# Kernel optimization log

Measured on AMD Instinct MI355X. Metric: run time of the kernel, lower is better.

## Reference

```python
import jax, jax.numpy as jnp
import numpy as np

# config
BSZ, L_, DM = 4, 2048, 1024
H, G, P, N, R = 16, 4, 64, 64, 2
RATIO = H // G            # 4
E, K = 64, 2              # kmoe experts / top_k
DPROJ = H * P * 2 + G * N * R * 2 + G * 3  # 3084


def rms(x, w, eps=1e-5):
    return x * jax.lax.rsqrt(jnp.mean(x * x, axis=-1, keepdims=True) + eps) * w


def kron_moe(x, router_w, A_e, B_e, scale, bias, d1, d2, o1, o2, k):
    # x: [..., d1*d2] -> [..., o1*o2]
    orig = x.shape
    xf = x.reshape(-1, d1 * d2)
    logits = xf @ router_w.T                       # [T, E]
    vals, idx = jax.lax.top_k(logits, k)           # [T, k]
    probs = jax.nn.softmax(vals, axis=-1)
    xs = xf.reshape(-1, d1, d2)
    # Y[t,k,o,p] = sum_ij A[t,k,o,i] x[t,i,j] B[t,k,p,j]
    Y = jnp.einsum('tkoi,tij,tkpj->tkop', A_e[idx], xs, B_e[idx])
    out = jnp.sum(Y * probs[:, :, None, None], axis=1).reshape(orig[:-1] + (o1 * o2,))
    return out * scale + bias


def setup_inputs() -> dict:
    key = jax.random.key(0)
    ks = jax.random.split(key, 12)
    r = lambda k, s, sc: jax.random.normal(k, s, jnp.float32) * sc
    return dict(
        u=jax.random.normal(ks[0], (BSZ, L_, DM), jnp.float32),
        in_proj_w=r(ks[1], (DPROJ, DM), 0.02),
        in_proj_b=jnp.zeros((DPROJ,), jnp.float32),
        xup_router=r(ks[2], (E, P), 0.02),
        xup_A=r(ks[3], (E, 8, 8), 0.1),
        xup_B=r(ks[4], (E, 16, 8), 0.1),
        xup_scale=jnp.ones((1,), jnp.float32),
        xup_bias=jnp.zeros((P * R,), jnp.float32),
        ydown_w=r(ks[5], (P, P * R), 0.02),
        oup_router=r(ks[6], (E, H * P), 0.02),
        oup_A=r(ks[7], (E, 32, 32), 0.05),
        oup_B=r(ks[8], (E, 32, 32), 0.05),
        oup_scale=jnp.ones((1,), jnp.float32),
        oup_bias=jnp.zeros((DM,), jnp.float32),
        theta_log=r(ks[9], (G, N // 2), 1.0),
        D=jnp.ones((H,), jnp.float32),
        normB_w=jnp.ones((N * R,), jnp.float32),
        normC_w=jnp.ones((N * R,), jnp.float32),
        bias_B=jnp.zeros((G, N, R), jnp.float32),
        bias_C=jnp.zeros((G, N, R), jnp.float32),
        pregate_w=jnp.ones((H * P,), jnp.float32),
    )


def reference(u, in_proj_w, in_proj_b, xup_router, xup_A, xup_B, xup_scale, xup_bias,
              ydown_w, oup_router, oup_A, oup_B, oup_scale, oup_bias,
              theta_log, D, normB_w, normC_w, bias_B, bias_C, pregate_w):
    B, L, _ = u.shape
    HP, GNR = H * P, G * N * R
    proj = u @ in_proj_w.T + in_proj_b
    splits = np.cumsum([HP, HP, GNR, GNR, G, G])
    z, x_p, Bp, Cp, dt, A_p, lam = jnp.split(proj, splits, axis=-1)
    dt = jax.nn.softplus(dt)                       # [B,L,G]
    A = -jnp.exp(A_p)                              # [B,L,G]
    theta = jnp.exp(theta_log)                     # [G,N/2]
    Bp = rms(Bp.reshape(B, L, G, N * R), normB_w).reshape(B, L, G, N, R) + bias_B
    Cp = rms(Cp.reshape(B, L, G, N * R), normC_w).reshape(B, L, G, N, R) + bias_C
    angles_g = jnp.cumsum(dt[..., None] * theta[None, None], axis=1)   # [B,L,G,N/2]
    rep = lambda v: jnp.repeat(v, RATIO, axis=2)   # group -> head broadcast
    angles = rep(angles_g)                         # [B,L,H,N/2]
    dt_h = rep(dt[..., None])                      # [B,L,H,1]
    A_h = rep(A[..., None])                        # [B,L,H,1]
    B_h, C_h = rep(Bp), rep(Cp)                    # [B,L,H,N,R]
    cos = jnp.cos(angles)[..., None]
    sin = jnp.sin(angles)[..., None]

    def rotate(v):
        re, im = v[..., 0::2, :], v[..., 1::2, :]
        return jnp.stack([re * cos - im * sin, re * sin + im * cos], axis=-2).reshape(v.shape)

    B_rot, C_rot = rotate(B_h), rotate(C_h)
    x = kron_moe(x_p.reshape(B, L, H, P), xup_router, xup_A, xup_B, xup_scale, xup_bias,
                 8, 8, 8, 16, K).reshape(B, L, H, P, R)
    alpha = jnp.exp(dt_h * A_h)[..., None]         # [B,L,H,1,1]

    mv = lambda v: jnp.moveaxis(v, 1, 0)           # time-major for scan

    def step(h, xs):
        Br, Cr, xt, at, dtt = xs
        in_sig = jnp.einsum('bhnr,bhpr->bhnp', Br, xt)
        h = h * at + dtt[..., None] * in_sig
        y_t = jnp.einsum('bhnp,bhnr->bhpr', h, Cr)
        return h, y_t

    h0 = jnp.zeros((B, H, N, P), u.dtype)
    _, ys = jax.lax.scan(step, h0, (mv(B_rot), mv(C_rot), mv(x), mv(alpha), mv(dt_h)))
    y = jnp.moveaxis(ys, 0, 1)                     # [B,L,H,P,R]
    y = (y.reshape(B, L, H, P * R) @ ydown_w.T).reshape(B, L, H * P)
    y = rms(y + x_p * jnp.repeat(D, P), pregate_w) * jax.nn.sigmoid(z)
    out = kron_moe(y, oup_router, oup_A, oup_B, oup_scale, oup_bias, 32, 32, 32, 32, K)
    return out
```

## Files before the change

kernel.cpp:

```cpp
#include <hip/hip_runtime.h>
#include <hip/hip_bf16.h>
#include <math.h>

namespace {
constexpr int kB = 4, kL = 2048, kDM = 1024;
constexpr int kH = 16, kG = 4;
constexpr int kDPROJ = 3084;
constexpr int COL_Z = 0, COL_XP = 1024, COL_B = 2048, COL_C = 2560, COL_DT = 3072, COL_A = 3076;
constexpr int kTOK = kB * kL;
constexpr int kNC = kL / 64;
constexpr int kNPAD = 3200;
constexpr float kLOG2E = 1.4426950408889634f;
}

typedef __attribute__((ext_vector_type(8))) __bf16 bf16x8;
typedef __attribute__((ext_vector_type(8))) unsigned short u16x8;
typedef __attribute__((ext_vector_type(4))) float f32x4;

#define GLDS16(gp, lp)                                                          \
  __builtin_amdgcn_global_load_lds(                                             \
      (const __attribute__((address_space(1))) void*)(gp),                      \
      (__attribute__((address_space(3))) void*)(lp), 16, 0, 0)

__device__ __forceinline__ unsigned short bf16_rne(float f) {
  unsigned u = __builtin_bit_cast(unsigned, f);
  unsigned r = u + 0x7fffu + ((u >> 16) & 1u);
  return (unsigned short)(r >> 16);
}
__device__ __forceinline__ void split2(float f, unsigned short& h, unsigned short& l) {
  unsigned short hh = bf16_rne(f);
  float hf = __builtin_bit_cast(float, (unsigned)hh << 16);
  h = hh;
  l = bf16_rne(f - hf);
}
__device__ __forceinline__ bf16x8 ldsb8(const unsigned short* p) {
  return __builtin_bit_cast(bf16x8, *(const u16x8*)p);
}

__global__ __launch_bounds__(256) void k_split_u(const float* __restrict__ X,
                                                 unsigned short* __restrict__ hi,
                                                 unsigned short* __restrict__ lo) {
  int i = blockIdx.x * 256 + threadIdx.x;
  float4 x = ((const float4*)X)[i];
  float xs[4] = {x.x, x.y, x.z, x.w};
  ushort4 hv, lv;
  unsigned short hq[4], lq[4];
#pragma unroll
  for (int q = 0; q < 4; ++q) split2(xs[q], hq[q], lq[q]);
  hv.x = hq[0]; hv.y = hq[1]; hv.z = hq[2]; hv.w = hq[3];
  lv.x = lq[0]; lv.y = lq[1]; lv.z = lq[2]; lv.w = lq[3];
  ((ushort4*)hi)[i] = hv;
  ((ushort4*)lo)[i] = lv;
}

__global__ __launch_bounds__(256) void k_split_w(const float* __restrict__ X,
                                                 unsigned short* __restrict__ hi,
                                                 unsigned short* __restrict__ lo) {
  int i = blockIdx.x * 256 + threadIdx.x;
  int row = i >> 8;
  float4 x = make_float4(0.f, 0.f, 0.f, 0.f);
  if (row < kDPROJ) x = ((const float4*)X)[i];
  float xs[4] = {x.x, x.y, x.z, x.w};
  ushort4 hv, lv;
  unsigned short hq[4], lq[4];
#pragma unroll
  for (int q = 0; q < 4; ++q) split2(xs[q], hq[q], lq[q]);
  hv.x = hq[0]; hv.y = hq[1]; hv.z = hq[2]; hv.w = hq[3];
  lv.x = lq[0]; lv.y = lq[1]; lv.z = lq[2]; lv.w = lq[3];
  ((ushort4*)hi)[i] = hv;
  ((ushort4*)lo)[i] = lv;
}

__global__ __launch_bounds__(256) void k_inproj_mfma(
    const unsigned short* __restrict__ Uhi, const unsigned short* __restrict__ Ulo,
    const unsigned short* __restrict__ Whi, const unsigned short* __restrict__ Wlo,
    const float* __restrict__ bias, float* __restrict__ proj,
    float* __restrict__ dtA) {
  __shared__ unsigned short lds_u[16384];
  const int tid = threadIdx.x;
  const int wave = tid >> 6, lane = tid & 63;
  const int wm = wave >> 1, wn = wave & 1;
  const int row0 = blockIdx.x * 128, col0 = blockIdx.y * 128;
  const int fr = lane & 15, kq = lane >> 4;

  f32x4 acc[4][4];
#pragma unroll
  for (int i = 0; i < 4; ++i)
#pragma unroll
    for (int j = 0; j < 4; ++j) acc[i][j] = (f32x4){0.f, 0.f, 0.f, 0.f};

  const int s0 = wave * 64 + lane;

  for (int k0 = 0; k0 < kDM; k0 += 32) {
#pragma unroll
    for (int q = 0; q < 2; ++q) {
      const int slot = q * 256 + s0;
      const int r = slot >> 2;
      const int ce = ((slot & 3) ^ ((r >> 1) & 3)) * 8;
      const size_t ao = (size_t)(row0 + r) * kDM + k0 + ce;
      const size_t bo = (size_t)(col0 + r) * kDM + k0 + ce;
      const int lb = (q * 256 + wave * 64) * 16;
      GLDS16(Uhi + ao, (char*)lds_u + lb);
      GLDS16(Ulo + ao, (char*)lds_u + 8192 + lb);
      GLDS16(Whi + bo, (char*)lds_u + 16384 + lb);
      GLDS16(Wlo + bo, (char*)lds_u + 24576 + lb);
    }
    __syncthreads();
    bf16x8 ahi[4], alo[4], bhi[4], blo[4];
#pragma unroll
    for (int mi = 0; mi < 4; ++mi) {
      int r = wm * 64 + mi * 16 + fr;
      int off = r * 32 + ((kq ^ ((r >> 1) & 3)) * 8);
      ahi[mi] = ldsb8(lds_u + off);
      alo[mi] = ldsb8(lds_u + 4096 + off);
    }
#pragma unroll
    for (int ni = 0; ni < 4; ++ni) {
      int r = wn * 64 + ni * 16 + fr;
      int off = r * 32 + ((kq ^ ((r >> 1) & 3)) * 8);
      bhi[ni] = ldsb8(lds_u + 8192 + off);
      blo[ni] = ldsb8(lds_u + 12288 + off);
    }
#pragma unroll
    for (int mi = 0; mi < 4; ++mi)
#pragma unroll
      for (int ni = 0; ni < 4; ++ni) {
        acc[mi][ni] = __builtin_amdgcn_mfma_f32_16x16x32_bf16(ahi[mi], bhi[ni], acc[mi][ni], 0, 0, 0);
        acc[mi][ni] = __builtin_amdgcn_mfma_f32_16x16x32_bf16(ahi[mi], blo[ni], acc[mi][ni], 0, 0, 0);
        acc[mi][ni] = __builtin_amdgcn_mfma_f32_16x16x32_bf16(alo[mi], bhi[ni], acc[mi][ni], 0, 0, 0);
      }
    __syncthreads();
  }

  const int orow = row0 + wm * 64, ocol = col0 + wn * 64;
#pragma unroll
  for (int mi = 0; mi < 4; ++mi)
#pragma unroll
    for (int ni = 0; ni < 4; ++ni) {
      int cg = ocol + ni * 16 + fr;
      if (cg < kDPROJ) {
        float bv = bias[cg];
#pragma unroll
        for (int r = 0; r < 4; ++r) {
          int rg = orow + mi * 16 + kq * 4 + r;
          float v = acc[mi][ni][r] + bv;
          proj[(size_t)rg * kDPROJ + cg] = v;
          if (cg >= COL_DT && cg < COL_DT + 8)
            dtA[(size_t)rg * 8 + (cg - COL_DT)] = v;
        }
      }
    }
}

__global__ __launch_bounds__(256) void k_dtprep(const float* __restrict__ dtA,
                                                float* __restrict__ dtg,
                                                float* __restrict__ cumalog,
                                                double* __restrict__ cumdt) {
  int bg = blockIdx.x;
  int b = bg / kG, g = bg % kG;
  int tid = threadIdx.x;
  __shared__ double s_dt[256], s_al[256];
  double loc_dt[8], loc_al[8];
  double sdt = 0.0, sal = 0.0;
#pragma unroll
  for (int q = 0; q < 8; ++q) {
    int t = tid * 8 + q;
    size_t i = (size_t)(b * kL + t) * 8;
    float rd = dtA[i + g];
    float ra = dtA[i + 4 + g];
    float dt = rd > 20.f ? rd : log1pf(expf(rd));
    float al = -expf(ra) * dt;
    dtg[(size_t)(b * kL + t) * kG + g] = dt;
    sdt += (double)dt; loc_dt[q] = sdt;
    sal += (double)al; loc_al[q] = sal;
  }
  s_dt[tid] = sdt; s_al[tid] = sal;
  __syncthreads();
  for (int off = 1; off < 256; off <<= 1) {
    double a = 0.0, c = 0.0;
    if (tid >= off) { a = s_dt[tid - off]; c = s_al[tid - off]; }
    __syncthreads();
    s_dt[tid] += a; s_al[tid] += c;
    __syncthreads();
  }
  double base_dt = tid ? s_dt[tid - 1] : 0.0;
  double base_al = tid ? s_al[tid - 1] : 0.0;
#pragma unroll
  for (int q = 0; q < 8; ++q) {
    int t = tid * 8 + q;
    size_t idx = (size_t)(b * kL + t) * kG + g;
    cumdt[idx] = base_dt + loc_dt[q];
    cumalog[idx] = (float)(base_al + loc_al[q]);
  }
}

__global__ __launch_bounds__(256) void k_angles(const double* __restrict__ cumdt,
                                                const float* __restrict__ theta_log,
                                                float* __restrict__ cs_tab) {
  int idx = blockIdx.x * 256 + threadIdx.x;
  int tok = idx >> 7, gk = idx & 127, g = gk >> 5, k = gk & 31;
  double theta = exp((double)theta_log[g * 32 + k]);
  double ang = theta * cumdt[(size_t)tok * kG + g];
  const double twopi = 6.283185307179586476925286766559;
  double rem = ang - floor(ang / twopi) * twopi;
  cs_tab[(size_t)idx * 2] = cosf((float)rem);
  cs_tab[(size_t)idx * 2 + 1] = sinf((float)rem);
}

__global__ __launch_bounds__(1024) void k_rotate(float* __restrict__ proj,
                                                 const float* __restrict__ cs_tab,
                                                 const float* __restrict__ normB_w,
                                                 const float* __restrict__ normC_w,
                                                 const float* __restrict__ bias_B,
                                                 const float* __restrict__ bias_C) {
  int tok = blockIdx.x;
  int tid = threadIdx.x;
  __shared__ float buf[1024];
  __shared__ float red[16];
  size_t rowoff = (size_t)tok * kDPROJ;
  int g = tid >> 8;
  int half = (tid >> 7) & 1;
  int j = tid & 127;
  int wave = tid >> 6;
  int col = (half ? COL_C : COL_B) + g * 128 + j;
  float v = proj[rowoff + col];
  float ss = v * v;
  for (int o = 1; o < 64; o <<= 1) ss += __shfl_xor(ss, o);
  if ((tid & 63) == 0) red[wave] = ss;
  __syncthreads();
  float tot = red[wave] + red[wave ^ 1];
  float scale = rsqrtf(tot / 128.f + 1e-5f);
  const float* nw = half ? normC_w : normB_w;
  const float* bb = half ? bias_C : bias_B;
  float nv = v * scale * nw[j] + bb[g * 128 + j];
  buf[tid] = nv;
  __syncthreads();
  float other = buf[tid ^ 2];
  int n = j >> 1;
  int k = n >> 1;
  bool isRe = (n & 1) == 0;
  const float* cs = cs_tab + (((size_t)tok * kG + g) * 32 + k) * 2;
  float cc = cs[0], sn = cs[1];
  float out = isRe ? (nv * cc - other * sn) : (other * sn + nv * cc);
  proj[rowoff + col] = out;
}

__global__ __launch_bounds__(256) void k_xlogits(const float* __restrict__ proj,
                                                 const float* __restrict__ router,
                                                 float* __restrict__ xroute) {
  __shared__ float Yt[16][65];
  __shared__ float Rt[64][65];
  __shared__ float cv[16][16][4];
  int tid = threadIdx.x;
  int tok = blockIdx.x;
  for (int m = tid; m < 1024; m += 256)
    Yt[m >> 6][m & 63] = proj[(size_t)tok * kDPROJ + COL_XP + m];
  for (int m = tid; m < 4096; m += 256)
    Rt[m >> 6][m & 63] = router[m];
  __syncthreads();
  int t = tid & 15;
  int grp = tid >> 4, e0 = grp * 4;
  float lg[4];
#pragma unroll
  for (int e = 0; e < 4; ++e) {
    double a0 = 0.0, a1 = 0.0, a2 = 0.0, a3 = 0.0;
#pragma unroll
    for (int d = 0; d < 64; d += 4) {
      a0 += (double)Rt[e0 + e][d + 0] * (double)Yt[t][d + 0];
      a1 += (double)Rt[e0 + e][d + 1] * (double)Yt[t][d + 1];
      a2 += (double)Rt[e0 + e][d + 2] * (double)Yt[t][d + 2];
      a3 += (double)Rt[e0 + e][d + 3] * (double)Yt[t][d + 3];
    }
    lg[e] = (float)((a0 + a1) + (a2 + a3));
  }
  float w1 = -INFINITY, w2 = -INFINITY; int j1 = 0, j2 = 0;
#pragma unroll
  for (int e = 0; e < 4; ++e) {
    float v = lg[e]; int idx = e0 + e;
    if (v > w1) { w2 = w1; j2 = j1; w1 = v; j1 = idx; }
    else if (v > w2) { w2 = v; j2 = idx; }
  }
  cv[t][grp][0] = w1; cv[t][grp][1] = __builtin_bit_cast(float, j1);
  cv[t][grp][2] = w2; cv[t][grp][3] = __builtin_bit_cast(float, j2);
  __syncthreads();
  if (tid < 16) {
    int tt = tid;
    float v1 = -INFINITY, v2 = -INFINITY; int i1 = 0, i2 = 0;
    for (int g = 0; g < 16; ++g) {
      float a = cv[tt][g][0]; int ai = __builtin_bit_cast(int, cv[tt][g][1]);
      if (a > v1) { v2 = v1; i2 = i1; v1 = a; i1 = ai; }
      else if (a > v2) { v2 = a; i2 = ai; }
      float b = cv[tt][g][2]; int bi = __builtin_bit_cast(int, cv[tt][g][3]);
      if (b > v1) { v2 = v1; i2 = i1; v1 = b; i1 = bi; }
      else if (b > v2) { v2 = b; i2 = bi; }
    }
    float e12 = expf(v2 - v1);
    float p1 = 1.f / (1.f + e12), p2 = e12 / (1.f + e12);
    float4 rt = make_float4(p1, p2, __builtin_bit_cast(float, i1),
                            __builtin_bit_cast(float, i2));
    *(float4*)&xroute[((size_t)tok * 16 + tt) * 4] = rt;
  }
}

__global__ __launch_bounds__(256) void k_xapply(const float* __restrict__ proj,
                                                const float* __restrict__ xroute,
                                                const float* __restrict__ Ae,
                                                const float* __restrict__ Be,
                                                const float* __restrict__ scale_,
                                                const float* __restrict__ bias_,
                                                float* __restrict__ xmoe) {
  int wave = threadIdx.x >> 6, lane = threadIdx.x & 63;
  int unit = blockIdx.x * 4 + wave;
  int tok = unit >> 4, h = unit & 15;
  const float4* xp4 = (const float4*)(proj + (size_t)tok * kDPROJ + COL_XP + h * 64);
  float4 xr[16];
#pragma unroll
  for (int i = 0; i < 16; ++i) xr[i] = xp4[i];
  float4 rt = *(const float4*)&xroute[(size_t)unit * 4];
  float p1 = rt.x, p2 = rt.y;
  int e1 = __builtin_amdgcn_readfirstlane(__builtin_bit_cast(int, rt.z));
  int e2 = __builtin_amdgcn_readfirstlane(__builtin_bit_cast(int, rt.w));
  const int p = lane & 15, o = lane >> 4;
  float out0 = 0.f, out1 = 0.f;
#pragma unroll
  for (int kk = 0; kk < 2; ++kk) {
    int e = kk ? e2 : e1;
    float pw = kk ? p2 : p1;
    const float4* Bp = (const float4*)(Be + (size_t)e * 128 + p * 8);
    float4 b0 = Bp[0], b1 = Bp[1];
    const float4* Ar = (const float4*)(Ae + (size_t)e * 64);
    float4 A0a = Ar[o * 2], A0b = Ar[o * 2 + 1];
    float4 A1a = Ar[(o + 4) * 2], A1b = Ar[(o + 4) * 2 + 1];
    float Ar0[8] = {A0a.x, A0a.y, A0a.z, A0a.w, A0b.x, A0b.y, A0b.z, A0b.w};
    float Ar1[8] = {A1a.x, A1a.y, A1a.z, A1a.w, A1b.x, A1b.y, A1b.z, A1b.w};
    float y0 = 0.f, y1 = 0.f;
#pragma unroll
    for (int i = 0; i < 8; ++i) {
      float4 xa = xr[i * 2], xb = xr[i * 2 + 1];
      float t = xa.x * b0.x + xa.y * b0.y + xa.z * b0.z + xa.w * b0.w
              + xb.x * b1.x + xb.y * b1.y + xb.z * b1.z + xb.w * b1.w;
      y0 += Ar0[i] * t;
      y1 += Ar1[i] * t;
    }
    out0 += pw * y0;
    out1 += pw * y1;
  }
  float sc = scale_[0];
  size_t ob = (size_t)unit * 128;
  xmoe[ob + lane] = out0 * sc + bias_[lane];
  xmoe[ob + lane + 64] = out1 * sc + bias_[lane + 64];
}

namespace { constexpr int SK = 136; }
__global__ __launch_bounds__(256) void k_passA(const float* __restrict__ proj,
                                               const float* __restrict__ xmoe,
                                               const float* __restrict__ dtg,
                                               const float* __restrict__ cumalog,
                                               float* __restrict__ hstate) {
  __shared__ unsigned short sBh[64 * SK];
  __shared__ unsigned short sBl[64 * SK];
  __shared__ unsigned short sXh[64 * SK];
  __shared__ unsigned short sXl[64 * SK];
  __shared__ float wv[64];
  int bid = blockIdx.x;
  int c = bid & 31, h = (bid >> 5) & 15, b = bid >> 9, g = h >> 2;
  int tid = threadIdx.x;
  const int wave = tid >> 6, lane = tid & 63;
  const int fr = lane & 15, kq = lane >> 4;
  int base = c * 64;
  size_t tok0 = (size_t)b * kL + base;
  if (tid < 64) {
    float ca_last = cumalog[(tok0 + 63) * kG + g];
    float ca_s = cumalog[(tok0 + tid) * kG + g];
    float dt = dtg[(tok0 + tid) * kG + g];
    wv[tid] = expf(ca_last - ca_s) * dt;
  }
  __syncthreads();
  for (int m = tid; m < 8192; m += 256) {
    int s = m >> 7, j = m & 127;
    int k = s * 2 + (j & 1), n = j >> 1;
    unsigned short hh, ll;
    float bval = proj[(tok0 + s) * kDPROJ + COL_B + g * 128 + j] * wv[s];
    split2(bval, hh, ll);
    sBh[n * SK + k] = hh; sBl[n * SK + k] = ll;
    float xval = xmoe[((tok0 + s) * kH + h) * (size_t)128 + j];
    split2(xval, hh, ll);
    sXh[n * SK + k] = hh; sXl[n * SK + k] = ll;
  }
  __syncthreads();
  const int n0 = wave * 16;
  f32x4 acc[4];
#pragma unroll
  for (int j = 0; j < 4; ++j) acc[j] = (f32x4){0.f, 0.f, 0.f, 0.f};
#pragma unroll
  for (int ks = 0; ks < 4; ++ks) {
    int kb = ks * 32 + kq * 8;
    int offA = (n0 + fr) * SK + kb;
    bf16x8 ah = ldsb8(sBh + offA);
    bf16x8 al = ldsb8(sBl + offA);
#pragma unroll
    for (int ni = 0; ni < 4; ++ni) {
      int offB = (ni * 16 + fr) * SK + kb;
      bf16x8 bh = ldsb8(sXh + offB);
      bf16x8 bl = ldsb8(sXl + offB);
      acc[ni] = __builtin_amdgcn_mfma_f32_16x16x32_bf16(ah, bh, acc[ni], 0, 0, 0);
      acc[ni] = __builtin_amdgcn_mfma_f32_16x16x32_bf16(ah, bl, acc[ni], 0, 0, 0);
      acc[ni] = __builtin_amdgcn_mfma_f32_16x16x32_bf16(al, bh, acc[ni], 0, 0, 0);
    }
  }
  float* out = hstate + (size_t)bid * 4096;
#pragma unroll
  for (int ni = 0; ni < 4; ++ni)
#pragma unroll
    for (int r = 0; r < 4; ++r) {
      int n = n0 + kq * 4 + r;
      int p = ni * 16 + fr;
      out[n * 64 + p] = acc[ni][r];
    }
}

__global__ __launch_bounds__(256) void k_passB(float* __restrict__ hstate,
                                               const float* __restrict__ cumalog) {
  int bid = blockIdx.x;
  int q8 = bid & 7, bh = bid >> 3;
  int b = bh >> 4, g = (bh & 15) >> 2;
  int tid = threadIdx.x;
  float hrun[2] = {0.f, 0.f};
  float* Hbase = hstate + (size_t)bh * 32 * 4096 + q8 * 512;
  for (int c = 0; c < 32; ++c) {
    float ca_last = cumalog[((size_t)b * kL + c * 64 + 63) * kG + g];
    float ca_prev = c ? cumalog[((size_t)b * kL + c * 64 - 1) * kG + g] : 0.f;
    float Dc = expf(ca_last - ca_prev);
    float* Hc = Hbase + (size_t)c * 4096;
#pragma unroll
    for (int q = 0; q < 2; ++q) {
      int idx = tid + q * 256;
      float local = Hc[idx];
      Hc[idx] = hrun[q];
      hrun[q] = Dc * hrun[q] + local;
    }
  }
}

namespace {
constexpr int SC = 72;
constexpr int SG = 136;
constexpr int SH = 72;
constexpr int SW = 66;
}
__global__ __launch_bounds__(1024) void k_passC(const float* __restrict__ proj,
                                                const float* __restrict__ xmoe,
                                                const float* __restrict__ dtg,
                                                const float* __restrict__ cumalog,
                                                const float* __restrict__ hstate,
                                                const float* __restrict__ ydown,
                                                float* __restrict__ outY) {
  __shared__ __align__(16) char smem[162560];
  unsigned short* sCh = (unsigned short*)smem;
  unsigned short* sCl = sCh + 128 * SC;
  unsigned short* sBh = (unsigned short*)(smem + 36864);
  unsigned short* sBl = sBh + 128 * SC;
  float*          sW  = (float*)(smem + 73728);
  unsigned short* sHh = (unsigned short*)(smem + 73728);
  unsigned short* sHl = sHh + 64 * SH;
  unsigned short* sGh = (unsigned short*)(smem + 92160);
  unsigned short* sGl = sGh + 128 * SG;
  float* sca  = (float*)(smem + 161792);
  float* sdts = sca + 64;
  float* selx = sdts + 64;
  unsigned short* sXh  = (unsigned short*)smem;
  unsigned short* sXl  = sXh + 64 * SG;
  unsigned short* sWdh = (unsigned short*)(smem + 36864);
  unsigned short* sWdl = sWdh + 64 * SG;
  unsigned short* sYh  = (unsigned short*)(smem + 92160);
  unsigned short* sYl  = sYh + 64 * SG;

  int bid = blockIdx.x;
  int c = bid & 31, h = (bid >> 5) & 15, b = bid >> 9, g = h >> 2;
  int tid = threadIdx.x;
  const int wave = tid >> 6, lane = tid & 63;
  const int fr = lane & 15, kq = lane >> 4;
  int base = c * 64;
  size_t tok0 = (size_t)b * kL + base;
  size_t projBase = tok0 * kDPROJ;

  if (tid < 64) {
    float ca_prev = base ? cumalog[(tok0 - 1) * kG + g] : 0.f;
    float ca_t = cumalog[(tok0 + tid) * kG + g];
    sca[tid] = ca_t;
    sdts[tid] = dtg[(tok0 + tid) * kG + g];
    selx[tid] = exp2f((ca_t - ca_prev) * kLOG2E);
  }
  for (int m = tid; m < 8192; m += 1024) {
    int s = m >> 7, j = m & 127;
    int row = s * 2 + (j & 1), col = j >> 1;
    unsigned short hh, ll;
    float cvv = proj[projBase + (size_t)s * kDPROJ + COL_C + g * 128 + j];
    split2(cvv, hh, ll);
    sCh[row * SC + col] = hh; sCl[row * SC + col] = ll;
    float bv = proj[projBase + (size_t)s * kDPROJ + COL_B + g * 128 + j];
    split2(bv, hh, ll);
    sBh[row * SC + col] = hh; sBl[row * SC + col] = ll;
  }
  __syncthreads();

  for (int m = tid; m < 4096; m += 1024) {
    int t = m >> 6, s = m & 63;
    float w = (s <= t) ? sdts[s] * exp2f((sca[t] - sca[s]) * kLOG2E) : 0.f;
    sW[t * SW + s] = w;
  }
  const int rowA0 = (wave & 7) * 16;
  const int colH = wave >> 3;
  f32x4 gacc[4];
#pragma unroll
  for (int j = 0; j < 4; ++j) gacc[j] = (f32x4){0.f, 0.f, 0.f, 0.f};
#pragma unroll
  for (int ks = 0; ks < 2; ++ks) {
    int kb = ks * 32 + kq * 8;
    int offA = (rowA0 + fr) * SC + kb;
    bf16x8 ah = ldsb8(sCh + offA);
    bf16x8 al = ldsb8(sCl + offA);
#pragma unroll
    for (int ni = 0; ni < 4; ++ni) {
      int off = (colH * 64 + ni * 16 + fr) * SC + kb;
      bf16x8 bh = ldsb8(sBh + off);
      bf16x8 bl = ldsb8(sBl + off);
      gacc[ni] = __builtin_amdgcn_mfma_f32_16x16x32_bf16(ah, bh, gacc[ni], 0, 0, 0);
      gacc[ni] = __builtin_amdgcn_mfma_f32_16x16x32_bf16(ah, bl, gacc[ni], 0, 0, 0);
      gacc[ni] = __builtin_amdgcn_mfma_f32_16x16x32_bf16(al, bh, gacc[ni], 0, 0, 0);
    }
  }
  __syncthreads();

#pragma unroll
  for (int ni = 0; ni < 4; ++ni) {
    int colg = colH * 64 + ni * 16 + fr;
    int s = colg >> 1;
#pragma unroll
    for (int r = 0; r < 4; ++r) {
      int rowg = rowA0 + kq * 4 + r;
      int t = rowg >> 1;
      float gm = gacc[ni][r] * sW[t * SW + s];
      unsigned short hh, ll;
      split2(gm, hh, ll);
      sGh[rowg * SG + colg] = hh;
      sGl[rowg * SG + colg] = ll;
    }
  }
  __syncthreads();

  for (int m = tid; m < 4096; m += 1024) {
    int n = m >> 6, p = m & 63;
    float v = hstate[(size_t)bid * 4096 + m];
    unsigned short hh, ll;
    split2(v, hh, ll);
    sHh[p * SH + n] = hh;
    sHl[p * SH + n] = ll;
  }
  __syncthreads();

  f32x4 yac[2];
#pragma unroll
  for (int j = 0; j < 2; ++j) yac[j] = (f32x4){0.f, 0.f, 0.f, 0.f};
#pragma unroll
  for (int ks = 0; ks < 2; ++ks) {
    int kb = ks * 32 + kq * 8;
    int offA = (rowA0 + fr) * SC + kb;
    bf16x8 ah = ldsb8(sCh + offA);
    bf16x8 al = ldsb8(sCl + offA);
#pragma unroll
    for (int ni = 0; ni < 2; ++ni) {
      int off = (colH * 32 + ni * 16 + fr) * SH + kb;
      bf16x8 bh = ldsb8(sHh + off);
      bf16x8 bl = ldsb8(sHl + off);
      yac[ni] = __builtin_amdgcn_mfma_f32_16x16x32_bf16(ah, bh, yac[ni], 0, 0, 0);
      yac[ni] = __builtin_amdgcn_mfma_f32_16x16x32_bf16(ah, bl, yac[ni], 0, 0, 0);
      yac[ni] = __builtin_amdgcn_mfma_f32_16x16x32_bf16(al, bh, yac[ni], 0, 0, 0);
    }
  }
#pragma unroll
  for (int r = 0; r < 4; ++r) {
    int t = (rowA0 + kq * 4 + r) >> 1;
    float e = selx[t];
#pragma unroll
    for (int ni = 0; ni < 2; ++ni) yac[ni][r] *= e;
  }
  __syncthreads();

  for (int m = tid; m < 8192; m += 1024) {
    int s = m >> 7, j = m & 127;
    float xv = xmoe[((tok0 + s) * kH + h) * (size_t)128 + j];
    int p = j >> 1, cc = s * 2 + (j & 1);
    unsigned short hh, ll;
    split2(xv, hh, ll);
    sXh[p * SG + cc] = hh; sXl[p * SG + cc] = ll;
    float wv2 = ydown[m];
    split2(wv2, hh, ll);
    sWdh[(m >> 7) * SG + (m & 127)] = hh;
    sWdl[(m >> 7) * SG + (m & 127)] = ll;
  }
  __syncthreads();

#pragma unroll
  for (int ks = 0; ks < 4; ++ks) {
    int kb = ks * 32 + kq * 8;
    int offA = (rowA0 + fr) * SG + kb;
    bf16x8 ah = ldsb8(sGh + offA);
    bf16x8 al = ldsb8(sGl + offA);
#pragma unroll
    for (int ni = 0; ni < 2; ++ni) {
      int off = (colH * 32 + ni * 16 + fr) * SG + kb;
      bf16x8 bh = ldsb8(sXh + off);
      bf16x8 bl = ldsb8(sXl + off);
      yac[ni] = __builtin_amdgcn_mfma_f32_16x16x32_bf16(ah, bh, yac[ni], 0, 0, 0);
      yac[ni] = __builtin_amdgcn_mfma_f32_16x16x32_bf16(ah, bl, yac[ni], 0, 0, 0);
      yac[ni] = __builtin_amdgcn_mfma_f32_16x16x32_bf16(al, bh, yac[ni], 0, 0, 0);
    }
  }
  __syncthreads();

#pragma unroll
  for (int ni = 0; ni < 2; ++ni)
#pragma unroll
    for (int r = 0; r < 4; ++r) {
      int rowg = rowA0 + kq * 4 + r;
      int t = rowg >> 1, rr = rowg & 1;
      int p = colH * 32 + ni * 16 + fr;
      unsigned short hh, ll;
      split2(yac[ni][r], hh, ll);
      sYh[t * SG + p * 2 + rr] = hh;
      sYl[t * SG + p * 2 + rr] = ll;
    }
  __syncthreads();

  f32x4 zac = (f32x4){0.f, 0.f, 0.f, 0.f};
  const int zr0 = (wave & 3) * 16, zc0 = (wave >> 2) * 16;
#pragma unroll
  for (int ks = 0; ks < 4; ++ks) {
    int kb = ks * 32 + kq * 8;
    int offA = (zr0 + fr) * SG + kb;
    bf16x8 ah = ldsb8(sYh + offA);
    bf16x8 al = ldsb8(sYl + offA);
    int offB = (zc0 + fr) * SG + kb;
    bf16x8 bh = ldsb8(sWdh + offB);
    bf16x8 bl = ldsb8(sWdl + offB);
    zac = __builtin_amdgcn_mfma_f32_16x16x32_bf16(ah, bh, zac, 0, 0, 0);
    zac = __builtin_amdgcn_mfma_f32_16x16x32_bf16(ah, bl, zac, 0, 0, 0);
    zac = __builtin_amdgcn_mfma_f32_16x16x32_bf16(al, bh, zac, 0, 0, 0);
  }
#pragma unroll
  for (int r = 0; r < 4; ++r) {
    int t = zr0 + kq * 4 + r;
    int o = zc0 + fr;
    outY[(tok0 + t) * (size_t)1024 + h * 64 + o] = zac[r];
  }
}

__global__ __launch_bounds__(256) void k_gate(float* __restrict__ y,
                                              const float* __restrict__ proj,
                                              const float* __restrict__ Dv,
                                              const float* __restrict__ pregate_w) {
  int tok = blockIdx.x;
  int tid = threadIdx.x;
  size_t yoff = (size_t)tok * 1024;
  size_t poff = (size_t)tok * kDPROJ;
  __shared__ float red[4];
  float vals[4];
  float ss = 0.f;
#pragma unroll
  for (int q = 0; q < 4; ++q) {
    int j = tid + q * 256;
    float v = y[yoff + j] + proj[poff + COL_XP + j] * Dv[j >> 6];
    vals[q] = v;
    ss += v * v;
  }
  for (int o = 1; o < 64; o <<= 1) ss += __shfl_xor(ss, o);
  if ((tid & 63) == 0) red[tid >> 6] = ss;
  __syncthreads();
  float tot = red[0] + red[1] + red[2] + red[3];
  float scale = rsqrtf(tot / 1024.f + 1e-5f);
#pragma unroll
  for (int q = 0; q < 4; ++q) {
    int j = tid + q * 256;
    float z = proj[poff + COL_Z + j];
    float sig = 1.f / (1.f + expf(-z));
    y[yoff + j] = vals[q] * scale * pregate_w[j] * sig;
  }
}

__global__ __launch_bounds__(256) void k_logits(const float* __restrict__ y,
                                                const float* __restrict__ router,
                                                float* __restrict__ oroute) {
  __shared__ float Yt[16][65];
  __shared__ float Rt[64][65];
  __shared__ float cv[16][16][4];
  int tid = threadIdx.x;
  int tok0 = blockIdx.x * 16;
  int t = tid & 15;
  int grp = tid >> 4, e0 = grp * 4;
  double acc[4] = {0.0, 0.0, 0.0, 0.0};
  for (int kc = 0; kc < 1024; kc += 64) {
    for (int m = tid; m < 1024; m += 256) {
      int tt = m >> 6, c = m & 63;
      Yt[tt][c] = y[(size_t)(tok0 + tt) * 1024 + kc + c];
    }
    for (int m = tid; m < 4096; m += 256) {
      int ee = m >> 6, c = m & 63;
      Rt[ee][c] = router[(size_t)ee * 1024 + kc + c];
    }
    __syncthreads();
    for (int c = 0; c < 64; ++c) {
      float yv = Yt[t][c];
#pragma unroll
      for (int i = 0; i < 4; ++i)
        acc[i] += (double)Rt[e0 + i][c] * (double)yv;
    }
    __syncthreads();
  }
  float w1 = -INFINITY, w2 = -INFINITY; int j1 = 0, j2 = 0;
#pragma unroll
  for (int e = 0; e < 4; ++e) {
    float v = (float)acc[e]; int idx = e0 + e;
    if (v > w1) { w2 = w1; j2 = j1; w1 = v; j1 = idx; }
    else if (v > w2) { w2 = v; j2 = idx; }
  }
  cv[t][grp][0] = w1; cv[t][grp][1] = __builtin_bit_cast(float, j1);
  cv[t][grp][2] = w2; cv[t][grp][3] = __builtin_bit_cast(float, j2);
  __syncthreads();
  if (tid < 16) {
    int tt = tid;
    float v1 = -INFINITY, v2 = -INFINITY; int i1 = 0, i2 = 0;
    for (int g = 0; g < 16; ++g) {
      float a = cv[tt][g][0]; int ai = __builtin_bit_cast(int, cv[tt][g][1]);
      if (a > v1) { v2 = v1; i2 = i1; v1 = a; i1 = ai; }
      else if (a > v2) { v2 = a; i2 = ai; }
      float b = cv[tt][g][2]; int bi = __builtin_bit_cast(int, cv[tt][g][3]);
      if (b > v1) { v2 = v1; i2 = i1; v1 = b; i1 = bi; }
      else if (b > v2) { v2 = b; i2 = bi; }
    }
    float e12 = expf(v2 - v1);
    float p1 = 1.f / (1.f + e12), p2 = e12 / (1.f + e12);
    float4 rt = make_float4(p1, p2, __builtin_bit_cast(float, i1),
                            __builtin_bit_cast(float, i2));
    *(float4*)&oroute[(size_t)(tok0 + tt) * 4] = rt;
  }
}

__global__ __launch_bounds__(256) void k_oup(float* __restrict__ y,
                                             const float* __restrict__ oroute,
                                             const float* __restrict__ Ae,
                                             const float* __restrict__ Be,
                                             const float* __restrict__ scale_,
                                             const float* __restrict__ bias_) {
  int tok = blockIdx.x;
  int tid = threadIdx.x;
  __shared__ float xs[1024];
  __shared__ float Ts[32][33];
  size_t yoff = (size_t)tok * 1024;
  for (int m = tid; m < 1024; m += 256) xs[m] = y[yoff + m];
  float4 rt = *(const float4*)&oroute[(size_t)tok * 4];
  float p1 = rt.x, p2 = rt.y;
  int i1 = __builtin_bit_cast(int, rt.z);
  int i2 = __builtin_bit_cast(int, rt.w);
  __syncthreads();
  float out[4] = {0.f, 0.f, 0.f, 0.f};
  for (int kk = 0; kk < 2; ++kk) {
    int e = kk ? i2 : i1;
    float pw = kk ? p2 : p1;
    const float* A = Ae + (size_t)e * 1024;
    const float* Bm = Be + (size_t)e * 1024;
    __syncthreads();
    for (int m = tid; m < 1024; m += 256) {
      int i = m >> 5, p = m & 31;
      float t = 0.f;
#pragma unroll
      for (int j = 0; j < 32; ++j) t += xs[i * 32 + j] * Bm[p * 32 + j];
      Ts[i][p] = t;
    }
    __syncthreads();
#pragma unroll
    for (int q = 0; q < 4; ++q) {
      int cc = tid + q * 256;
      int o = cc >> 5, p = cc & 31;
      float a2 = 0.f;
#pragma unroll
      for (int i = 0; i < 32; ++i) a2 += A[o * 32 + i] * Ts[i][p];
      out[q] += pw * a2;
    }
  }
  float sc = scale_[0];
#pragma unroll
  for (int q = 0; q < 4; ++q) {
    int cc = tid + q * 256;
    y[yoff + cc] = out[q] * sc + bias_[cc];
  }
}

extern "C" void kernel_launch(void* const* d_in, const int* in_sizes, int n_in,
                              void* d_out, int out_size, void* d_ws, size_t ws_size,
                              hipStream_t stream) {
  const float* u          = (const float*)d_in[0];
  const float* in_proj_w  = (const float*)d_in[1];
  const float* in_proj_b  = (const float*)d_in[2];
  const float* xup_router = (const float*)d_in[3];
  const float* xup_A      = (const float*)d_in[4];
  const float* xup_B      = (const float*)d_in[5];
  const float* xup_scale  = (const float*)d_in[6];
  const float* xup_bias   = (const float*)d_in[7];
  const float* ydown_w    = (const float*)d_in[8];
  const float* oup_router = (const float*)d_in[9];
  const float* oup_A      = (const float*)d_in[10];
  const float* oup_B      = (const float*)d_in[11];
  const float* oup_scale  = (const float*)d_in[12];
  const float* oup_bias   = (const float*)d_in[13];
  const float* theta_log  = (const float*)d_in[14];
  const float* Dv         = (const float*)d_in[15];
  const float* normB_w    = (const float*)d_in[16];
  const float* normC_w    = (const float*)d_in[17];
  const float* bias_B     = (const float*)d_in[18];
  const float* bias_C     = (const float*)d_in[19];
  const float* pregate_w  = (const float*)d_in[20];

  char* ws = (char*)d_ws;
  float* proj = (float*)ws;      ws += (size_t)kTOK * kDPROJ * 4;
  float* dtg = (float*)ws;       ws += (size_t)kTOK * kG * 4;
  float* cumalog = (float*)ws;   ws += (size_t)kTOK * kG * 4;
  double* cumdt = (double*)ws;   ws += (size_t)kTOK * kG * 8;
  float* dtA = (float*)ws;       ws += (size_t)kTOK * 8 * 4;
  float* cs_tab = (float*)ws;    ws += (size_t)kTOK * kG * 32 * 2 * 4;
  float* xmoe = (float*)ws;      ws += (size_t)kTOK * kH * 128 * 4;
  float* hstate = (float*)ws;    ws += (size_t)kB * kH * kNC * 4096 * 4;
  float* outY = (float*)d_out;

  float* xroute = cs_tab;
  float* oroute = cs_tab + 524288;

  unsigned short* Uhi = (unsigned short*)xmoe;
  unsigned short* Ulo = Uhi + (size_t)kTOK * kDM;
  unsigned short* Whi = Ulo + (size_t)kTOK * kDM;
  unsigned short* Wlo = Whi + (size_t)kNPAD * kDM;

  k_split_u<<<dim3(kTOK * kDM / 4 / 256), dim3(256), 0, stream>>>(u, Uhi, Ulo);
  k_split_w<<<dim3(kNPAD * kDM / 4 / 256), dim3(256), 0, stream>>>(in_proj_w, Whi, Wlo);
  k_inproj_mfma<<<dim3(kTOK / 128, kNPAD / 128), dim3(256), 0, stream>>>(Uhi, Ulo, Whi, Wlo, in_proj_b, proj, dtA);
  k_dtprep<<<dim3(kB * kG), dim3(256), 0, stream>>>(dtA, dtg, cumalog, cumdt);
  k_angles<<<dim3(kTOK * 128 / 256), dim3(256), 0, stream>>>(cumdt, theta_log, cs_tab);
  k_rotate<<<dim3(kTOK), dim3(1024), 0, stream>>>(proj, cs_tab, normB_w, normC_w, bias_B, bias_C);
  k_xlogits<<<dim3(kTOK), dim3(256), 0, stream>>>(proj, xup_router, xroute);
  k_xapply<<<dim3(kTOK * kH / 4), dim3(256), 0, stream>>>(proj, xroute, xup_A, xup_B, xup_scale, xup_bias, xmoe);
  k_passA<<<dim3(kB * kH * kNC), dim3(256), 0, stream>>>(proj, xmoe, dtg, cumalog, hstate);
  k_passB<<<dim3(kB * kH * 8), dim3(256), 0, stream>>>(hstate, cumalog);
  k_passC<<<dim3(kB * kH * kNC), dim3(1024), 0, stream>>>(proj, xmoe, dtg, cumalog, hstate, ydown_w, outY);
  k_gate<<<dim3(kTOK), dim3(256), 0, stream>>>(outY, proj, Dv, pregate_w);
  k_logits<<<dim3(kTOK / 16), dim3(256), 0, stream>>>(outY, oup_router, oroute);
  k_oup<<<dim3(kTOK), dim3(256), 0, stream>>>(outY, oroute, oup_A, oup_B, oup_scale, oup_bias);
}
```

Baseline: 1.032 ms.

## Batch two tokens per xup-router block and move top-2 selection into apply

The xup router logits kernel now handles two tokens per block with register-blocked double-precision dot products, so each loaded router value is reused across two units and the router tile is loaded half as often. It writes raw logits into the hstate workspace instead of doing the top-2 reduction through shared memory. The top-2 selection and softmax move into k_xapply as a 64-lane wave shuffle reduction. In exchange, 64 logits per unit make a round trip through global memory, and the shuffle reduction adds work to the apply kernel. Ties now go to the lower expert index, which may differ from the earlier selection logic.

```diff
diff --git a/kernel.cpp b/kernel.cpp
--- a/kernel.cpp
+++ b/kernel.cpp
@@ -247,63 +247,58 @@
 
 __global__ __launch_bounds__(256) void k_xlogits(const float* __restrict__ proj,
                                                  const float* __restrict__ router,
-                                                 float* __restrict__ xroute) {
-  __shared__ float Yt[16][65];
+                                                 float* __restrict__ logits) {
+  __shared__ float Yt[32][65];
   __shared__ float Rt[64][65];
-  __shared__ float cv[16][16][4];
   int tid = threadIdx.x;
-  int tok = blockIdx.x;
-  for (int m = tid; m < 1024; m += 256)
-    Yt[m >> 6][m & 63] = proj[(size_t)tok * kDPROJ + COL_XP + m];
+  int tok0 = blockIdx.x * 2;
+  for (int m = tid; m < 2048; m += 256) {
+    int t = m >> 10, off = m & 1023;
+    Yt[t * 16 + (off >> 6)][off & 63] = proj[(size_t)(tok0 + t) * kDPROJ + COL_XP + off];
+  }
   for (int m = tid; m < 4096; m += 256)
     Rt[m >> 6][m & 63] = router[m];
   __syncthreads();
-  int t = tid & 15;
-  int grp = tid >> 4, e0 = grp * 4;
-  float lg[4];
-#pragma unroll
-  for (int e = 0; e < 4; ++e) {
-    double a0 = 0.0, a1 = 0.0, a2 = 0.0, a3 = 0.0;
-#pragma unroll
-    for (int d = 0; d < 64; d += 4) {
-      a0 += (double)Rt[e0 + e][d + 0] * (double)Yt[t][d + 0];
-      a1 += (double)Rt[e0 + e][d + 1] * (double)Yt[t][d + 1];
-      a2 += (double)Rt[e0 + e][d + 2] * (double)Yt[t][d + 2];
-      a3 += (double)Rt[e0 + e][d + 3] * (double)Yt[t][d + 3];
-    }
-    lg[e] = (float)((a0 + a1) + (a2 + a3));
-  }
-  float w1 = -INFINITY, w2 = -INFINITY; int j1 = 0, j2 = 0;
-#pragma unroll
-  for (int e = 0; e < 4; ++e) {
-    float v = lg[e]; int idx = e0 + e;
-    if (v > w1) { w2 = w1; j2 = j1; w1 = v; j1 = idx; }
-    else if (v > w2) { w2 = v; j2 = idx; }
-  }
-  cv[t][grp][0] = w1; cv[t][grp][1] = __builtin_bit_cast(float, j1);
-  cv[t][grp][2] = w2; cv[t][grp][3] = __builtin_bit_cast(float, j2);
-  __syncthreads();
-  if (tid < 16) {
-    int tt = tid;
-    float v1 = -INFINITY, v2 = -INFINITY; int i1 = 0, i2 = 0;
-    for (int g = 0; g < 16; ++g) {
-      float a = cv[tt][g][0]; int ai = __builtin_bit_cast(int, cv[tt][g][1]);
-      if (a > v1) { v2 = v1; i2 = i1; v1 = a; i1 = ai; }
-      else if (a > v2) { v2 = a; i2 = ai; }
-      float b = cv[tt][g][2]; int bi = __builtin_bit_cast(int, cv[tt][g][3]);
-      if (b > v1) { v2 = v1; i2 = i1; v1 = b; i1 = bi; }
-      else if (b > v2) { v2 = b; i2 = bi; }
-    }
-    float e12 = expf(v2 - v1);
-    float p1 = 1.f / (1.f + e12), p2 = e12 / (1.f + e12);
-    float4 rt = make_float4(p1, p2, __builtin_bit_cast(float, i1),
-                            __builtin_bit_cast(float, i2));
-    *(float4*)&xroute[((size_t)tok * 16 + tt) * 4] = rt;
-  }
+  const int up = tid & 15;
+  const int e0 = (tid >> 4) * 4;
+  double acc[2][4][4];
+#pragma unroll
+  for (int ui = 0; ui < 2; ++ui)
+#pragma unroll
+    for (int e = 0; e < 4; ++e)
+#pragma unroll
+      for (int gq = 0; gq < 4; ++gq) acc[ui][e][gq] = 0.0;
+#pragma unroll
+  for (int d0 = 0; d0 < 64; d0 += 8) {
+    double yd[2][8];
+#pragma unroll
+    for (int ui = 0; ui < 2; ++ui)
+#pragma unroll
+      for (int dd = 0; dd < 8; ++dd)
+        yd[ui][dd] = (double)Yt[up * 2 + ui][d0 + dd];
+#pragma unroll
+    for (int e = 0; e < 4; ++e) {
+      double rd[8];
+#pragma unroll
+      for (int dd = 0; dd < 8; ++dd) rd[dd] = (double)Rt[e0 + e][d0 + dd];
+#pragma unroll
+      for (int ui = 0; ui < 2; ++ui)
+#pragma unroll
+        for (int dd = 0; dd < 8; ++dd)
+          acc[ui][e][dd & 3] += rd[dd] * yd[ui][dd];
+    }
+  }
+#pragma unroll
+  for (int ui = 0; ui < 2; ++ui)
+#pragma unroll
+    for (int e = 0; e < 4; ++e) {
+      float lg = (float)((acc[ui][e][0] + acc[ui][e][1]) + (acc[ui][e][2] + acc[ui][e][3]));
+      logits[(size_t)(tok0 * 16 + up * 2 + ui) * 64 + e0 + e] = lg;
+    }
 }
 
 __global__ __launch_bounds__(256) void k_xapply(const float* __restrict__ proj,
-                                                const float* __restrict__ xroute,
+                                                const float* __restrict__ logits,
                                                 const float* __restrict__ Ae,
                                                 const float* __restrict__ Be,
                                                 const float* __restrict__ scale_,
@@ -316,10 +311,22 @@
   float4 xr[16];
 #pragma unroll
   for (int i = 0; i < 16; ++i) xr[i] = xp4[i];
-  float4 rt = *(const float4*)&xroute[(size_t)unit * 4];
-  float p1 = rt.x, p2 = rt.y;
-  int e1 = __builtin_amdgcn_readfirstlane(__builtin_bit_cast(int, rt.z));
-  int e2 = __builtin_amdgcn_readfirstlane(__builtin_bit_cast(int, rt.w));
+  float logit = logits[(size_t)unit * 64 + lane];
+  float v1 = logit; int i1 = lane;
+  for (int o = 1; o < 64; o <<= 1) {
+    float vv = __shfl_xor(v1, o); int ii = __shfl_xor(i1, o);
+    if (vv > v1 || (vv == v1 && ii < i1)) { v1 = vv; i1 = ii; }
+  }
+  float lm = (lane == i1) ? -INFINITY : logit;
+  float v2 = lm; int i2 = lane;
+  for (int o = 1; o < 64; o <<= 1) {
+    float vv = __shfl_xor(v2, o); int ii = __shfl_xor(i2, o);
+    if (vv > v2 || (vv == v2 && ii < i2)) { v2 = vv; i2 = ii; }
+  }
+  int e1 = __builtin_amdgcn_readfirstlane(i1);
+  int e2 = __builtin_amdgcn_readfirstlane(i2);
+  float e12 = expf(v2 - v1);
+  float p1 = 1.f / (1.f + e12), p2 = e12 / (1.f + e12);
   const int p = lane & 15, o = lane >> 4;
   float out0 = 0.f, out1 = 0.f;
 #pragma unroll
@@ -832,8 +839,8 @@
   float* hstate = (float*)ws;    ws += (size_t)kB * kH * kNC * 4096 * 4;
   float* outY = (float*)d_out;
 
-  float* xroute = cs_tab;
-  float* oroute = cs_tab + 524288;
+  float* logits_x = hstate;
+  float* oroute = cs_tab;
 
   unsigned short* Uhi = (unsigned short*)xmoe;
   unsigned short* Ulo = Uhi + (size_t)kTOK * kDM;
@@ -846,8 +853,8 @@
   k_dtprep<<<dim3(kB * kG), dim3(256), 0, stream>>>(dtA, dtg, cumalog, cumdt);
   k_angles<<<dim3(kTOK * 128 / 256), dim3(256), 0, stream>>>(cumdt, theta_log, cs_tab);
   k_rotate<<<dim3(kTOK), dim3(1024), 0, stream>>>(proj, cs_tab, normB_w, normC_w, bias_B, bias_C);
-  k_xlogits<<<dim3(kTOK), dim3(256), 0, stream>>>(proj, xup_router, xroute);
-  k_xapply<<<dim3(kTOK * kH / 4), dim3(256), 0, stream>>>(proj, xroute, xup_A, xup_B, xup_scale, xup_bias, xmoe);
+  k_xlogits<<<dim3(kTOK / 2), dim3(256), 0, stream>>>(proj, xup_router, logits_x);
+  k_xapply<<<dim3(kTOK * kH / 4), dim3(256), 0, stream>>>(proj, logits_x, xup_A, xup_B, xup_scale, xup_bias, xmoe);
   k_passA<<<dim3(kB * kH * kNC), dim3(256), 0, stream>>>(proj, xmoe, dtg, cumalog, hstate);
   k_passB<<<dim3(kB * kH * 8), dim3(256), 0, stream>>>(hstate, cumalog);
   k_passC<<<dim3(kB * kH * kNC), dim3(1024), 0, stream>>>(proj, xmoe, dtg, cumalog, hstate, ydown_w, outY);
```

New measurement: 952.8 us. -7.6%, faster.
